# Kernel optimization log

Hardware: AMD Instinct MI355X
Metric: run time of the kernel (lower is better)

Reference implementation:

```python
import jax, jax.numpy as jnp
import numpy as np

B, N, C, H = 16, 4096, 256, 4
D = C // H


def setup_inputs() -> dict:
    key = jax.random.key(0)
    ks = jax.random.split(key, 16)
    s = 0.02
    inp = {
        "x": jax.random.normal(ks[0], (B, N, C), jnp.float32),
        "encoding": jax.random.normal(ks[1], (2, B, 1, N, D), jnp.float32),
        "Wqkv_w": jax.random.normal(ks[2], (3 * C, C), jnp.float32) * s,
        "Wqkv_b": jnp.zeros((3 * C,), jnp.float32),
        "tssa_qkv_w": jax.random.normal(ks[3], (C, C), jnp.float32) * s,
        "tssa_qkv_b": jnp.zeros((C,), jnp.float32),
        "temp": jnp.ones((H, 1), jnp.float32),
        "tssa_out_w": jax.random.normal(ks[4], (C, C), jnp.float32) * s,
        "tssa_out_b": jnp.zeros((C,), jnp.float32),
        "out_proj_w": jax.random.normal(ks[5], (C, C), jnp.float32) * s,
        "out_proj_b": jnp.zeros((C,), jnp.float32),
        "ffn1_w": jax.random.normal(ks[6], (2 * C, 2 * C), jnp.float32) * s,
        "ffn1_b": jnp.zeros((2 * C,), jnp.float32),
        "ln_g": jnp.ones((2 * C,), jnp.float32),
        "ln_b": jnp.zeros((2 * C,), jnp.float32),
        "ffn2_w": jax.random.normal(ks[7], (C, 2 * C), jnp.float32) * s,
        "ffn2_b": jnp.zeros((C,), jnp.float32),
    }
    return inp


def _rotate_half(t):
    # (..., d) -> pairwise rotate: (x1, x2) -> (-x2, x1)
    t2 = t.reshape(t.shape[:-1] + (-1, 2))
    x1, x2 = t2[..., 0], t2[..., 1]
    return jnp.stack((-x2, x1), axis=-1).reshape(t.shape)


def reference(x, encoding, Wqkv_w, Wqkv_b, tssa_qkv_w, tssa_qkv_b, temp,
              tssa_out_w, tssa_out_b, out_proj_w, out_proj_b,
              ffn1_w, ffn1_b, ln_g, ln_b, ffn2_w, ffn2_b):
    b, n, c = x.shape
    h, d = H, D
    # QKV projection, layout (h, d, 3) on last dim as in unflatten(-1,(h,-1,3))
    qkv = (x @ Wqkv_w.T + Wqkv_b).reshape(b, n, h, d, 3).transpose(0, 2, 1, 3, 4)  # b h n d 3
    q, k, v = qkv[..., 0], qkv[..., 1], qkv[..., 2]
    rope = lambda t: t * encoding[0] + _rotate_half(t) * encoding[1]
    q = rope(q)
    k = rope(k)
    flat = lambda t: t.transpose(0, 2, 1, 3).reshape(b, n, c)  # b h n d -> b n (h d)
    w_input = (flat(q) + flat(k) + flat(v)) / 3.0
    # TSSA attention
    w = (w_input @ tssa_qkv_w.T + tssa_qkv_b).reshape(b, n, h, d).transpose(0, 2, 1, 3)  # b h n d
    norm = jnp.sqrt(jnp.sum(w * w, axis=2, keepdims=True))  # L2 over sequence axis N
    w_normed = w / jnp.maximum(norm, 1e-12)
    sum_ws = jnp.sum(w_normed * w_normed, axis=-1)  # b h n
    Pi = jax.nn.softmax(sum_ws * temp[None, :, :], axis=1)  # softmax over heads
    Pi_norm = Pi / (jnp.sum(Pi, axis=-1, keepdims=True) + 1e-8)
    dots = jnp.einsum('bhn,bhnd->bh', Pi_norm, w * w)  # (b,h,1,d) summed over d
    attn = 1.0 / (1.0 + dots)  # b h
    out = -(w * Pi[..., None]) * attn[:, :, None, None]  # b h n d
    out = out.transpose(0, 2, 1, 3).reshape(b, n, c)
    context = out @ tssa_out_w.T + tssa_out_b
    message = context @ out_proj_w.T + out_proj_b
    # residual FFN
    cat = jnp.concatenate([x, message], axis=-1)  # b n 2c
    h1 = cat @ ffn1_w.T + ffn1_b
    mu = jnp.mean(h1, axis=-1, keepdims=True)
    var = jnp.mean((h1 - mu) ** 2, axis=-1, keepdims=True)
    ln = (h1 - mu) / jnp.sqrt(var + 1e-5) * ln_g + ln_b
    g = jax.nn.gelu(ln, approximate=False)
    return x + (g @ ffn2_w.T + ffn2_b)
```

## Files before the change

### kernel.cpp

```cpp
#include <hip/hip_runtime.h>
#include <math.h>

#define Bc 16
#define Nc 4096

typedef __attribute__((ext_vector_type(8))) short short8;
typedef __attribute__((ext_vector_type(4))) float floatx4;

__device__ __forceinline__ unsigned short f2bf(float f) {
    union { float f; unsigned int u; } v; v.f = f;
    unsigned int u = v.u;
    return (unsigned short)((u + 0x7fffu + ((u >> 16) & 1u)) >> 16);
}
__device__ __forceinline__ float bf2f(unsigned short u) {
    union { unsigned int u; float f; } v; v.u = ((unsigned int)u) << 16;
    return v.f;
}

__device__ __forceinline__ float gelu_f(float x) {
    const float z = x * 0.70710678118654752f;
    const float az = fabsf(z);
    const float t = 1.f / (1.f + 0.3275911f * az);
    const float poly = t * (0.254829592f + t * (-0.284496736f +
                       t * (1.421413741f + t * (-1.453152027f + t * 1.061405429f))));
    const float e = __expf(-z * z);
    const float er = copysignf(1.f - poly * e, z);
    return 0.5f * x * (1.f + er);
}

__device__ __forceinline__ void gll16(const unsigned short* g, unsigned short* l) {
    __builtin_amdgcn_global_load_lds(
        (const __attribute__((address_space(1))) void*)g,
        (__attribute__((address_space(3))) void*)l,
        16, 0, 0);
}

template <int EPI, typename TOUT>
__global__ __launch_bounds__(512) void gemm_bf(
    const unsigned short* __restrict__ A0, int lda0,
    const unsigned short* __restrict__ A1, int lda1, int K0,
    const unsigned short* __restrict__ W,
    const float* __restrict__ bias,
    const unsigned short* __restrict__ resid_bf,
    const float* __restrict__ Pi,
    const float* __restrict__ Sb,
    const float* __restrict__ Tb,
    float* __restrict__ norm2,
    float* __restrict__ rowstats,
    const float* __restrict__ enc,
    const float* __restrict__ lng,
    const float* __restrict__ lnb,
    TOUT* __restrict__ C, int N, int K)
{
    __shared__ alignas(16) unsigned short As[128 * 64];
    __shared__ alignas(16) unsigned short Bs[256 * 64];

    const int t = threadIdx.x;
    const int bn = blockIdx.x, bm = blockIdx.y;
    const int lane = t & 63, wave = t >> 6;
    const int wm = wave >> 2, wn = wave & 3;
    const int quad = lane >> 4, l16 = lane & 15;
    const int rt = t >> 3, st = t & 7;

    float mean0 = 0.f, rstd0 = 0.f, mean1 = 0.f, rstd1 = 0.f;
    if constexpr (EPI == 3) {
        const size_t g0 = (size_t)bm * 128 + rt;
        const float2 s0 = *(const float2*)(rowstats + g0 * 2);
        const float2 s1 = *(const float2*)(rowstats + (g0 + 64) * 2);
        mean0 = s0.x * (1.f / 512.f);
        rstd0 = rsqrtf(s0.y * (1.f / 512.f) - mean0 * mean0 + 1e-5f);
        mean1 = s1.x * (1.f / 512.f);
        rstd1 = rsqrtf(s1.y * (1.f / 512.f) - mean1 * mean1 + 1e-5f);
    }

    floatx4 acc[4][4];
    #pragma unroll
    for (int i = 0; i < 4; ++i)
        #pragma unroll
        for (int j = 0; j < 4; ++j)
            acc[i][j] = (floatx4){0.f, 0.f, 0.f, 0.f};

    for (int k0 = 0; k0 < K; k0 += 64) {
        #pragma unroll
        for (int hh = 0; hh < 2; ++hh) {
            const int row = hh * 64 + rt;
            const int col = k0 + (st ^ (row & 7)) * 8;
            unsigned short* ldsa = As + row * 64 + st * 8;
            const size_t grow = (size_t)bm * 128 + row;
            if constexpr (EPI == 6) {
                if (k0 < K0) {
                    gll16(A0 + grow * (size_t)lda0 + col, ldsa);
                } else {
                    const int b = (int)(grow >> 12);
                    const int hd = (col - K0) >> 6;
                    const float Sv = Sb[b * 4 + hd], Tv = Tb[b * 4 + hd];
                    const float at = 1.f / (1.f + Tv / (Sv + 1e-8f));
                    const float sc = -Pi[grow * 4 + hd] * at;
                    const short8 a = *(const short8*)(A1 + grow * (size_t)lda1 + (col - K0));
                    short8 o;
                    #pragma unroll
                    for (int j = 0; j < 8; ++j) o[j] = (short)f2bf(bf2f((unsigned short)a[j]) * sc);
                    *(short8*)ldsa = o;
                }
            } else if constexpr (EPI == 3) {
                const float mean = hh ? mean1 : mean0;
                const float rstd = hh ? rstd1 : rstd0;
                const short8 a = *(const short8*)(A0 + grow * (size_t)lda0 + col);
                const float4 ga = *(const float4*)(lng + col);
                const float4 gb = *(const float4*)(lng + col + 4);
                const float4 ba = *(const float4*)(lnb + col);
                const float4 bb = *(const float4*)(lnb + col + 4);
                const float vg[8] = {ga.x, ga.y, ga.z, ga.w, gb.x, gb.y, gb.z, gb.w};
                const float vb[8] = {ba.x, ba.y, ba.z, ba.w, bb.x, bb.y, bb.z, bb.w};
                short8 o;
                #pragma unroll
                for (int jj = 0; jj < 8; ++jj) {
                    const float ln = (bf2f((unsigned short)a[jj]) - mean) * rstd * vg[jj] + vb[jj];
                    o[jj] = (short)f2bf(gelu_f(ln));
                }
                *(short8*)ldsa = o;
            } else {
                const unsigned short* src = (col < K0)
                    ? (A0 + grow * (size_t)lda0 + col)
                    : (A1 + grow * (size_t)lda1 + (col - K0));
                gll16(src, ldsa);
            }
        }
        #pragma unroll
        for (int hh = 0; hh < 4; ++hh) {
            const int row = hh * 64 + rt;
            const int col = k0 + (st ^ (row & 7)) * 8;
            gll16(W + ((size_t)bn * 256 + row) * (size_t)K + col, Bs + row * 64 + st * 8);
        }
        __syncthreads();
        #pragma unroll
        for (int kk = 0; kk < 2; ++kk) {
            short8 af[4], wf[4];
            #pragma unroll
            for (int i = 0; i < 4; ++i) {
                const int ra = wm * 64 + i * 16 + l16;
                af[i] = *(const short8*)(As + ra * 64 + ((quad + kk * 4) ^ (ra & 7)) * 8);
                const int rw = wn * 64 + i * 16 + l16;
                wf[i] = *(const short8*)(Bs + rw * 64 + ((quad + kk * 4) ^ (rw & 7)) * 8);
            }
            #pragma unroll
            for (int mi = 0; mi < 4; ++mi)
                #pragma unroll
                for (int ni = 0; ni < 4; ++ni)
                    acc[mi][ni] = __builtin_amdgcn_mfma_f32_16x16x32_bf16(
                        wf[ni], af[mi], acc[mi][ni], 0, 0, 0);
        }
        __syncthreads();
    }

    float rs[4], rq[4];
    if constexpr (EPI == 6) {
        #pragma unroll
        for (int m = 0; m < 4; ++m) { rs[m] = 0.f; rq[m] = 0.f; }
    }

    #pragma unroll
    for (int mi = 0; mi < 4; ++mi) {
        const size_t row = (size_t)bm * 128 + wm * 64 + mi * 16 + l16;
        #pragma unroll
        for (int ni = 0; ni < 4; ++ni) {
            const int cb = bn * 256 + wn * 64 + ni * 16 + quad * 4;
            const float4 b4 = *(const float4*)(bias + cb);
            if constexpr (EPI == 5) {
                const float s0 = acc[mi][ni][0] + b4.x;
                const float v0 = acc[mi][ni][1] + b4.y;
                const float s1 = acc[mi][ni][2] + b4.z;
                const float v1 = acc[mi][ni][3] + b4.w;
                const int j = cb >> 1;
                const int d = j & 63;
                const float2 e0 = *(const float2*)(enc + row * 64 + d);
                const float2 e1 = *(const float2*)(enc + 4194304 + row * 64 + d);
                const float r0 = s0 * e0.x - s1 * e1.x;
                const float r1 = s1 * e0.y + s0 * e1.y;
                ushort2 o;
                o.x = f2bf((r0 + v0) * (1.f / 3.f));
                o.y = f2bf((r1 + v1) * (1.f / 3.f));
                *(ushort2*)((unsigned short*)C + row * (size_t)N + j) = o;
            } else {
                float v[4] = {acc[mi][ni][0] + b4.x, acc[mi][ni][1] + b4.y,
                              acc[mi][ni][2] + b4.z, acc[mi][ni][3] + b4.w};
                if constexpr (EPI == 3) {
                    const ushort4 xr = *(const ushort4*)(resid_bf + row * (size_t)N + cb);
                    v[0] += bf2f(xr.x); v[1] += bf2f(xr.y);
                    v[2] += bf2f(xr.z); v[3] += bf2f(xr.w);
                }
                if constexpr (EPI == 6) {
                    #pragma unroll
                    for (int rg = 0; rg < 4; ++rg) { rs[mi] += v[rg]; rq[mi] += v[rg] * v[rg]; }
                }
                if constexpr (EPI == 1) {
                    float cs[4];
                    #pragma unroll
                    for (int rg = 0; rg < 4; ++rg) cs[rg] = v[rg] * v[rg];
                    #pragma unroll
                    for (int rg = 0; rg < 4; ++rg) {
                        float s = cs[rg];
                        s += __shfl_xor(s, 1, 64);
                        s += __shfl_xor(s, 2, 64);
                        s += __shfl_xor(s, 4, 64);
                        s += __shfl_xor(s, 8, 64);
                        if (l16 == 0) atomicAdd(&norm2[(bm >> 5) * 256 + cb + rg], s);
                    }
                }
                if constexpr (__is_same(TOUT, float)) {
                    float4 o; o.x = v[0]; o.y = v[1]; o.z = v[2]; o.w = v[3];
                    *(float4*)(C + row * (size_t)N + cb) = o;
                } else {
                    ushort4 o;
                    o.x = f2bf(v[0]); o.y = f2bf(v[1]); o.z = f2bf(v[2]); o.w = f2bf(v[3]);
                    *(ushort4*)(C + row * (size_t)N + cb) = o;
                }
            }
        }
    }
    if constexpr (EPI == 6) {
        #pragma unroll
        for (int mi = 0; mi < 4; ++mi) {
            float s = rs[mi], q = rq[mi];
            s += __shfl_xor(s, 16, 64); s += __shfl_xor(s, 32, 64);
            q += __shfl_xor(q, 16, 64); q += __shfl_xor(q, 32, 64);
            if (quad == 0) {
                const size_t row = (size_t)bm * 128 + wm * 64 + mi * 16 + l16;
                atomicAdd(&rowstats[row * 2], s);
                atomicAdd(&rowstats[row * 2 + 1], q);
            }
        }
    }
}

__device__ __forceinline__ void conv8(const float* src, unsigned short* dst, int i) {
    const float4 f0 = *(const float4*)(src + (size_t)i * 8);
    const float4 f1 = *(const float4*)(src + (size_t)i * 8 + 4);
    short8 sv;
    sv[0] = (short)f2bf(f0.x); sv[1] = (short)f2bf(f0.y);
    sv[2] = (short)f2bf(f0.z); sv[3] = (short)f2bf(f0.w);
    sv[4] = (short)f2bf(f1.x); sv[5] = (short)f2bf(f1.y);
    sv[6] = (short)f2bf(f1.z); sv[7] = (short)f2bf(f1.w);
    *(short8*)(dst + (size_t)i * 8) = sv;
}

__global__ __launch_bounds__(256) void prep_all(
    const float* __restrict__ x, const float* __restrict__ Wqkv,
    const float* __restrict__ bqkv, const float* __restrict__ tssa_w,
    const float* __restrict__ op_w, const float* __restrict__ to_w,
    const float* __restrict__ to_b, const float* __restrict__ op_b,
    const float* __restrict__ f1w, const float* __restrict__ f2w,
    unsigned short* __restrict__ x_bf, unsigned short* __restrict__ Wsv,
    float* __restrict__ bsv, unsigned short* __restrict__ tssa_bf,
    unsigned short* __restrict__ Wf, float* __restrict__ bfb,
    unsigned short* __restrict__ ffn1_bf, unsigned short* __restrict__ ffn2_bf,
    float* __restrict__ zbase, float* __restrict__ rowstats)
{
    const int blk = blockIdx.x, tt = threadIdx.x;
    if (blk < 8192) {
        conv8(x, x_bf, blk * 256 + tt);
    } else if (blk < 8704) {
        const int r = blk - 8192, c = tt;
        const int j = r >> 1;
        const int h = j >> 6, dd = j & 63;
        const int base = h * 192 + dd * 3;
        if (!(r & 1)) {
            Wsv[r * 256 + c] = f2bf(Wqkv[(base + 0) * 256 + c] + Wqkv[(base + 1) * 256 + c]);
            if (c == 0) bsv[r] = bqkv[base] + bqkv[base + 1];
        } else {
            Wsv[r * 256 + c] = f2bf(Wqkv[(base + 2) * 256 + c]);
            if (c == 0) bsv[r] = bqkv[base + 2];
        }
    } else if (blk < 8960) {
        const int i = blk - 8704;
        float s = 0.f;
        for (int k = 0; k < 256; ++k) s += op_w[i * 256 + k] * to_w[k * 256 + tt];
        Wf[i * 256 + tt] = f2bf(s);
    } else if (blk == 8960) {
        float s = op_b[tt];
        for (int k = 0; k < 256; ++k) s += op_w[tt * 256 + k] * to_b[k];
        bfb[tt] = s;
    } else if (blk < 8993) {
        conv8(tssa_w, tssa_bf, (blk - 8961) * 256 + tt);
    } else if (blk < 9121) {
        conv8(f1w, ffn1_bf, (blk - 8993) * 256 + tt);
    } else if (blk < 9185) {
        conv8(f2w, ffn2_bf, (blk - 9121) * 256 + tt);
    } else {
        const int i = (blk - 9185) * 256 + tt;
        if (i < 4288) zbase[i] = 0.f;
        else if (i < 135360) rowstats[i - 4288] = 0.f;
    }
}

__global__ __launch_bounds__(256) void prep2(
    const float* __restrict__ f1w,
    const float* __restrict__ f1b,
    const unsigned short* __restrict__ Wf,
    const float* __restrict__ bfb,
    unsigned short* __restrict__ ffn1_bf,
    float* __restrict__ cbias)
{
    const int j = blockIdx.x, k = threadIdx.x;
    float s = 0.f;
    for (int i = 0; i < 256; ++i)
        s += f1w[(size_t)j * 512 + 256 + i] * bf2f(Wf[i * 256 + k]);
    ffn1_bf[(size_t)j * 512 + 256 + k] = f2bf(s);
    if (k == 0) {
        float c = f1b[j];
        for (int i = 0; i < 256; ++i) c += f1w[(size_t)j * 512 + 256 + i] * bfb[i];
        cbias[j] = c;
    }
}

__global__ __launch_bounds__(256) void pi_kernel(const unsigned short* __restrict__ w,
                                                 const float* __restrict__ norm2,
                                                 const float* __restrict__ temp,
                                                 float* __restrict__ Pi,
                                                 float* __restrict__ S,
                                                 float* __restrict__ T) {
    const int t = threadIdx.x;
    const int i = t & 15;
    const int lr = t >> 4;
    const size_t r = (size_t)blockIdx.x * 16 + lr;
    const int b = (int)(r >> 12);
    const unsigned short* wrow = w + r * 256;
    const float* n2row = norm2 + b * 256;
    float raw[4], nrm[4];
    #pragma unroll
    for (int h = 0; h < 4; ++h) {
        const ushort4 wv = *(const ushort4*)(wrow + h * 64 + i * 4);
        const float w0 = bf2f(wv.x), w1 = bf2f(wv.y), w2 = bf2f(wv.z), w3 = bf2f(wv.w);
        const float4 n2 = *(const float4*)(n2row + h * 64 + i * 4);
        const float s0 = w0 * w0, s1 = w1 * w1, s2 = w2 * w2, s3 = w3 * w3;
        raw[h] = s0 + s1 + s2 + s3;
        nrm[h] = s0 / fmaxf(n2.x, 1e-24f) + s1 / fmaxf(n2.y, 1e-24f)
               + s2 / fmaxf(n2.z, 1e-24f) + s3 / fmaxf(n2.w, 1e-24f);
    }
    #pragma unroll
    for (int off = 1; off < 16; off <<= 1) {
        #pragma unroll
        for (int h = 0; h < 4; ++h) {
            raw[h] += __shfl_xor(raw[h], off, 64);
            nrm[h] += __shfl_xor(nrm[h], off, 64);
        }
    }
    float sw[4], m = -1e30f;
    #pragma unroll
    for (int h = 0; h < 4; ++h) { sw[h] = nrm[h] * temp[h]; m = fmaxf(m, sw[h]); }
    float e[4], Z = 0.f;
    #pragma unroll
    for (int h = 0; h < 4; ++h) { e[h] = expf(sw[h] - m); Z += e[h]; }
    const float invZ = 1.f / Z;
    float pi[4];
    #pragma unroll
    for (int h = 0; h < 4; ++h) pi[h] = e[h] * invZ;
    if (i < 4) Pi[r * 4 + i] = pi[i];

    __shared__ float sS[16][4], sT[16][4];
    if (i == 0) {
        #pragma unroll
        for (int h = 0; h < 4; ++h) { sS[lr][h] = pi[h]; sT[lr][h] = pi[h] * raw[h]; }
    }
    __syncthreads();
    if (t < 4) {
        float as = 0.f, at = 0.f;
        for (int rr = 0; rr < 16; ++rr) { as += sS[rr][t]; at += sT[rr][t]; }
        atomicAdd(&S[b * 4 + t], as);
        atomicAdd(&T[b * 4 + t], at);
    }
}

extern "C" void kernel_launch(void* const* d_in, const int* in_sizes, int n_in,
                              void* d_out, int out_size, void* d_ws, size_t ws_size,
                              hipStream_t stream) {
    (void)in_sizes; (void)n_in; (void)out_size; (void)ws_size;
    const float* x          = (const float*)d_in[0];
    const float* enc        = (const float*)d_in[1];
    const float* Wqkv_w     = (const float*)d_in[2];
    const float* Wqkv_b     = (const float*)d_in[3];
    const float* tssa_qkv_w = (const float*)d_in[4];
    const float* tssa_qkv_b = (const float*)d_in[5];
    const float* temp       = (const float*)d_in[6];
    const float* tssa_out_w = (const float*)d_in[7];
    const float* tssa_out_b = (const float*)d_in[8];
    const float* out_proj_w = (const float*)d_in[9];
    const float* out_proj_b = (const float*)d_in[10];
    const float* ffn1_w     = (const float*)d_in[11];
    const float* ffn1_b     = (const float*)d_in[12];
    const float* ln_g       = (const float*)d_in[13];
    const float* ln_b       = (const float*)d_in[14];
    const float* ffn2_w     = (const float*)d_in[15];
    const float* ffn2_b     = (const float*)d_in[16];
    float* outp = (float*)d_out;

    const int M = Bc * Nc;

    char* ws = (char*)d_ws;
    unsigned short* x_bf  = (unsigned short*)(ws);
    unsigned short* wi_bf = (unsigned short*)(ws + (size_t)(32 << 20));
    unsigned short* h1_bf = (unsigned short*)(ws + (size_t)(32 << 20));
    unsigned short* w_bf  = (unsigned short*)(ws + (size_t)(64 << 20));
    float* fb    = (float*)(ws + (size_t)(128 << 20));
    float* Pi    = fb;
    float* norm2 = Pi + 262144;
    float* Sb    = norm2 + 4096;
    float* Tb    = Sb + 64;
    float* cbias = Tb + 64;
    float* bsv   = cbias + 512;
    float* bfb   = bsv + 512;
    float* rowstats = bfb + 256;
    unsigned short* Wsv_bf  = (unsigned short*)(rowstats + 131072);
    unsigned short* tssa_bf = Wsv_bf + 131072;
    unsigned short* Wf_bf   = tssa_bf + 65536;
    unsigned short* ffn1_bf = Wf_bf + 65536;
    unsigned short* ffn2_bf = ffn1_bf + 262144;

    prep_all<<<9714, 256, 0, stream>>>(
        x, Wqkv_w, Wqkv_b, tssa_qkv_w, out_proj_w, tssa_out_w, tssa_out_b,
        out_proj_b, ffn1_w, ffn2_w,
        x_bf, Wsv_bf, bsv, tssa_bf, Wf_bf, bfb, ffn1_bf, ffn2_bf,
        norm2, rowstats);

    prep2<<<512, 256, 0, stream>>>(ffn1_w, ffn1_b, Wf_bf, bfb, ffn1_bf, cbias);

    gemm_bf<5, unsigned short><<<dim3(2, M / 128), 512, 0, stream>>>(
        x_bf, 256, x_bf, 256, 256, Wsv_bf, bsv,
        nullptr, nullptr, nullptr, nullptr, nullptr, nullptr,
        enc, nullptr, nullptr, wi_bf, 256, 256);

    gemm_bf<1, unsigned short><<<dim3(1, M / 128), 512, 0, stream>>>(
        wi_bf, 256, wi_bf, 256, 256, tssa_bf, tssa_qkv_b,
        nullptr, nullptr, nullptr, nullptr, norm2, nullptr,
        nullptr, nullptr, nullptr, w_bf, 256, 256);

    pi_kernel<<<4096, 256, 0, stream>>>(w_bf, norm2, temp, Pi, Sb, Tb);

    gemm_bf<6, unsigned short><<<dim3(2, M / 128), 512, 0, stream>>>(
        x_bf, 256, w_bf, 256, 256, ffn1_bf, cbias,
        nullptr, Pi, Sb, Tb, nullptr, rowstats,
        nullptr, nullptr, nullptr, h1_bf, 512, 512);

    gemm_bf<3, float><<<dim3(1, M / 128), 512, 0, stream>>>(
        h1_bf, 512, h1_bf, 512, 512, ffn2_bf, ffn2_b,
        x_bf, nullptr, nullptr, nullptr, nullptr, rowstats,
        nullptr, ln_g, ln_b, outp, 256, 512);
}
```

Baseline: 482.4 us.

## Prefetch register-transformed A tiles two stages ahead and template K dimensions

Result: slower. 503.4 us (+4.3%).

```diff
diff --git a/kernel.cpp b/kernel.cpp
--- a/kernel.cpp
+++ b/kernel.cpp
@@ -35,10 +35,10 @@
         16, 0, 0);
 }
 
-template <int EPI, typename TOUT>
-__global__ __launch_bounds__(512) void gemm_bf(
+template <int EPI, int KT, int K0T, typename TOUT>
+__global__ __launch_bounds__(512, 4) void gemm_bf(
     const unsigned short* __restrict__ A0, int lda0,
-    const unsigned short* __restrict__ A1, int lda1, int K0,
+    const unsigned short* __restrict__ A1, int lda1,
     const unsigned short* __restrict__ W,
     const float* __restrict__ bias,
     const unsigned short* __restrict__ resid_bf,
@@ -50,8 +50,10 @@
     const float* __restrict__ enc,
     const float* __restrict__ lng,
     const float* __restrict__ lnb,
-    TOUT* __restrict__ C, int N, int K)
+    TOUT* __restrict__ C, int N)
 {
+    constexpr int NT = KT / 64;
+    constexpr bool REG = (EPI == 3) || (EPI == 6);
     __shared__ alignas(16) unsigned short As[128 * 64];
     __shared__ alignas(16) unsigned short Bs[256 * 64];
 
@@ -62,17 +64,76 @@
     const int quad = lane >> 4, l16 = lane & 15;
     const int rt = t >> 3, st = t & 7;
 
+    const int colin = (st ^ (rt & 7)) * 8;
+    const size_t g0 = (size_t)bm * 128 + rt;
+    const size_t g1 = g0 + 64;
+
     float mean0 = 0.f, rstd0 = 0.f, mean1 = 0.f, rstd1 = 0.f;
     if constexpr (EPI == 3) {
-        const size_t g0 = (size_t)bm * 128 + rt;
         const float2 s0 = *(const float2*)(rowstats + g0 * 2);
-        const float2 s1 = *(const float2*)(rowstats + (g0 + 64) * 2);
+        const float2 s1 = *(const float2*)(rowstats + g1 * 2);
         mean0 = s0.x * (1.f / 512.f);
         rstd0 = rsqrtf(s0.y * (1.f / 512.f) - mean0 * mean0 + 1e-5f);
         mean1 = s1.x * (1.f / 512.f);
         rstd1 = rsqrtf(s1.y * (1.f / 512.f) - mean1 * mean1 + 1e-5f);
     }
 
+    float sc[2][4];
+    if constexpr (EPI == 6) {
+        const int b = (bm * 128) >> 12;
+        const floatx4 Sv = *(const floatx4*)(Sb + b * 4);
+        const floatx4 Tv = *(const floatx4*)(Tb + b * 4);
+        const floatx4 p0 = *(const floatx4*)(Pi + g0 * 4);
+        const floatx4 p1 = *(const floatx4*)(Pi + g1 * 4);
+        #pragma unroll
+        for (int h = 0; h < 4; ++h) {
+            const float at = 1.f / (1.f + Tv[h] / (Sv[h] + 1e-8f));
+            sc[0][h] = -p0[h] * at;
+            sc[1][h] = -p1[h] * at;
+        }
+    }
+
+    short8 pa[2][2];
+    auto loadA = [&](int tt, int slot) {
+        const int cc = tt * 64 + colin;
+        if constexpr (EPI == 6) {
+            pa[slot][0] = *(const short8*)(A1 + g0 * (size_t)lda1 + (cc - K0T));
+            pa[slot][1] = *(const short8*)(A1 + g1 * (size_t)lda1 + (cc - K0T));
+        } else {
+            pa[slot][0] = *(const short8*)(A0 + g0 * (size_t)lda0 + cc);
+            pa[slot][1] = *(const short8*)(A0 + g1 * (size_t)lda0 + cc);
+        }
+    };
+    auto xform = [&](int tt, int slot) {
+        #pragma unroll
+        for (int hh = 0; hh < 2; ++hh) {
+            unsigned short* ldsa = As + (hh * 64 + rt) * 64 + st * 8;
+            const short8 a = pa[slot][hh];
+            short8 o;
+            if constexpr (EPI == 6) {
+                const float s = sc[hh][tt - K0T / 64];
+                #pragma unroll
+                for (int j = 0; j < 8; ++j) o[j] = (short)f2bf(bf2f((unsigned short)a[j]) * s);
+            } else {
+                const float mu = hh ? mean1 : mean0;
+                const float rs_ = hh ? rstd1 : rstd0;
+                const int cc = tt * 64 + colin;
+                const float4 ga = *(const float4*)(lng + cc);
+                const float4 gb = *(const float4*)(lng + cc + 4);
+                const float4 ba = *(const float4*)(lnb + cc);
+                const float4 bb = *(const float4*)(lnb + cc + 4);
+                const float vg[8] = {ga.x, ga.y, ga.z, ga.w, gb.x, gb.y, gb.z, gb.w};
+                const float vb[8] = {ba.x, ba.y, ba.z, ba.w, bb.x, bb.y, bb.z, bb.w};
+                #pragma unroll
+                for (int j = 0; j < 8; ++j) {
+                    const float ln = (bf2f((unsigned short)a[j]) - mu) * rs_ * vg[j] + vb[j];
+                    o[j] = (short)f2bf(gelu_f(ln));
+                }
+            }
+            *(short8*)ldsa = o;
+        }
+    };
+
     floatx4 acc[4][4];
     #pragma unroll
     for (int i = 0; i < 4; ++i)
@@ -80,57 +141,39 @@
         for (int j = 0; j < 4; ++j)
             acc[i][j] = (floatx4){0.f, 0.f, 0.f, 0.f};
 
-    for (int k0 = 0; k0 < K; k0 += 64) {
-        #pragma unroll
-        for (int hh = 0; hh < 2; ++hh) {
-            const int row = hh * 64 + rt;
-            const int col = k0 + (st ^ (row & 7)) * 8;
-            unsigned short* ldsa = As + row * 64 + st * 8;
-            const size_t grow = (size_t)bm * 128 + row;
-            if constexpr (EPI == 6) {
-                if (k0 < K0) {
-                    gll16(A0 + grow * (size_t)lda0 + col, ldsa);
-                } else {
-                    const int b = (int)(grow >> 12);
-                    const int hd = (col - K0) >> 6;
-                    const float Sv = Sb[b * 4 + hd], Tv = Tb[b * 4 + hd];
-                    const float at = 1.f / (1.f + Tv / (Sv + 1e-8f));
-                    const float sc = -Pi[grow * 4 + hd] * at;
-                    const short8 a = *(const short8*)(A1 + grow * (size_t)lda1 + (col - K0));
-                    short8 o;
-                    #pragma unroll
-                    for (int j = 0; j < 8; ++j) o[j] = (short)f2bf(bf2f((unsigned short)a[j]) * sc);
-                    *(short8*)ldsa = o;
-                }
-            } else if constexpr (EPI == 3) {
-                const float mean = hh ? mean1 : mean0;
-                const float rstd = hh ? rstd1 : rstd0;
-                const short8 a = *(const short8*)(A0 + grow * (size_t)lda0 + col);
-                const float4 ga = *(const float4*)(lng + col);
-                const float4 gb = *(const float4*)(lng + col + 4);
-                const float4 ba = *(const float4*)(lnb + col);
-                const float4 bb = *(const float4*)(lnb + col + 4);
-                const float vg[8] = {ga.x, ga.y, ga.z, ga.w, gb.x, gb.y, gb.z, gb.w};
-                const float vb[8] = {ba.x, ba.y, ba.z, ba.w, bb.x, bb.y, bb.z, bb.w};
-                short8 o;
-                #pragma unroll
-                for (int jj = 0; jj < 8; ++jj) {
-                    const float ln = (bf2f((unsigned short)a[jj]) - mean) * rstd * vg[jj] + vb[jj];
-                    o[jj] = (short)f2bf(gelu_f(ln));
-                }
-                *(short8*)ldsa = o;
+    if constexpr (EPI == 3) { loadA(0, 0); loadA(1, 1); }
+
+    #pragma unroll
+    for (int tt = 0; tt < NT; ++tt) {
+        const int k0 = tt * 64;
+        if constexpr (EPI == 6) {
+            if (k0 < K0T) {
+                gll16(A0 + g0 * (size_t)lda0 + k0 + colin, As + rt * 64 + st * 8);
+                gll16(A0 + g1 * (size_t)lda0 + k0 + colin, As + (64 + rt) * 64 + st * 8);
             } else {
-                const unsigned short* src = (col < K0)
-                    ? (A0 + grow * (size_t)lda0 + col)
-                    : (A1 + grow * (size_t)lda1 + (col - K0));
-                gll16(src, ldsa);
+                xform(tt, tt & 1);
             }
-        }
-        #pragma unroll
-        for (int hh = 0; hh < 4; ++hh) {
-            const int row = hh * 64 + rt;
-            const int col = k0 + (st ^ (row & 7)) * 8;
-            gll16(W + ((size_t)bn * 256 + row) * (size_t)K + col, Bs + row * 64 + st * 8);
+        } else if constexpr (EPI == 3) {
+            xform(tt, tt & 1);
+        } else {
+            const unsigned short* s0 = (k0 < K0T)
+                ? (A0 + g0 * (size_t)lda0 + k0 + colin)
+                : (A1 + g0 * (size_t)lda1 + (k0 - K0T) + colin);
+            const unsigned short* s1 = (k0 < K0T)
+                ? (A0 + g1 * (size_t)lda0 + k0 + colin)
+                : (A1 + g1 * (size_t)lda1 + (k0 - K0T) + colin);
+            gll16(s0, As + rt * 64 + st * 8);
+            gll16(s1, As + (64 + rt) * 64 + st * 8);
+        }
+        #pragma unroll
+        for (int hh = 0; hh < 4; ++hh)
+            gll16(W + ((size_t)bn * 256 + hh * 64 + rt) * KT + k0 + colin,
+                  Bs + (hh * 64 + rt) * 64 + st * 8);
+        if constexpr (EPI == 3) {
+            if (tt + 2 < NT) loadA(tt + 2, tt & 1);
+        }
+        if constexpr (EPI == 6) {
+            if (tt + 2 < NT && (tt + 2) * 64 >= K0T) loadA(tt + 2, tt & 1);
         }
         __syncthreads();
         #pragma unroll
@@ -424,25 +467,25 @@
 
     prep2<<<512, 256, 0, stream>>>(ffn1_w, ffn1_b, Wf_bf, bfb, ffn1_bf, cbias);
 
-    gemm_bf<5, unsigned short><<<dim3(2, M / 128), 512, 0, stream>>>(
-        x_bf, 256, x_bf, 256, 256, Wsv_bf, bsv,
+    gemm_bf<5, 256, 256, unsigned short><<<dim3(2, M / 128), 512, 0, stream>>>(
+        x_bf, 256, x_bf, 256, Wsv_bf, bsv,
         nullptr, nullptr, nullptr, nullptr, nullptr, nullptr,
-        enc, nullptr, nullptr, wi_bf, 256, 256);
-
-    gemm_bf<1, unsigned short><<<dim3(1, M / 128), 512, 0, stream>>>(
-        wi_bf, 256, wi_bf, 256, 256, tssa_bf, tssa_qkv_b,
+        enc, nullptr, nullptr, wi_bf, 256);
+
+    gemm_bf<1, 256, 256, unsigned short><<<dim3(1, M / 128), 512, 0, stream>>>(
+        wi_bf, 256, wi_bf, 256, tssa_bf, tssa_qkv_b,
         nullptr, nullptr, nullptr, nullptr, norm2, nullptr,
-        nullptr, nullptr, nullptr, w_bf, 256, 256);
+        nullptr, nullptr, nullptr, w_bf, 256);
 
     pi_kernel<<<4096, 256, 0, stream>>>(w_bf, norm2, temp, Pi, Sb, Tb);
 
-    gemm_bf<6, unsigned short><<<dim3(2, M / 128), 512, 0, stream>>>(
-        x_bf, 256, w_bf, 256, 256, ffn1_bf, cbias,
+    gemm_bf<6, 512, 256, unsigned short><<<dim3(2, M / 128), 512, 0, stream>>>(
+        x_bf, 256, w_bf, 256, ffn1_bf, cbias,
         nullptr, Pi, Sb, Tb, nullptr, rowstats,
-        nullptr, nullptr, nullptr, h1_bf, 512, 512);
-
-    gemm_bf<3, float><<<dim3(1, M / 128), 512, 0, stream>>>(
-        h1_bf, 512, h1_bf, 512, 512, ffn2_bf, ffn2_b,
+        nullptr, nullptr, nullptr, h1_bf, 512);
+
+    gemm_bf<3, 512, 512, float><<<dim3(1, M / 128), 512, 0, stream>>>(
+        h1_bf, 512, h1_bf, 512, ffn2_bf, ffn2_b,
         x_bf, nullptr, nullptr, nullptr, nullptr, rowstats,
-        nullptr, ln_g, ln_b, outp, 256, 512);
-}
+        nullptr, ln_g, ln_b, outp, 256);
+}
```
